# Kernel tuning notes

Hardware: AMD Instinct MI355X
Metric: run time of the kernel (lower is better)

Reference implementation:

```python
import jax, jax.numpy as jnp
import numpy as np

B, L, H, LH = 512, 128, 768, 256  # batch, max_seq_len, bert hidden, lstm hidden


def setup_inputs() -> dict:
    key = jax.random.key(0)
    ks = jax.random.split(key, 12)
    def rn(k, shape, s=0.02):
        return jax.random.normal(k, shape, dtype=jnp.float32) * s
    return {
        "x": jax.random.normal(ks[0], (B, L, H), dtype=jnp.float32),  # summed BERT layers 8:
        "w_ih": rn(ks[1], (4 * LH, H)),
        "w_hh": rn(ks[2], (4 * LH, LH)),
        "b_ih": jnp.zeros((4 * LH,), jnp.float32),
        "b_hh": jnp.zeros((4 * LH,), jnp.float32),
        "conv1_w": rn(ks[3], (256, H, 7)),   # Conv2d(1,256,(7,768)) == 1D conv, in=768
        "conv1_b": jnp.zeros((256,), jnp.float32),
        "conv2_w": rn(ks[4], (64, 256, 5)),
        "conv2_b": jnp.zeros((64,), jnp.float32),
        "conv3_w": rn(ks[5], (256, 64, 3)),
        "conv3_b": jnp.zeros((256,), jnp.float32),
        "conv4_w": rn(ks[6], (16, 256, 1)),
        "conv4_b": jnp.zeros((16,), jnp.float32),
        "fc1_w": rn(ks[7], (128, LH + 2 * L)),  # lstm_hidden + cnn_feature_size
        "fc1_b": jnp.zeros((128,), jnp.float32),
        "fc2_w": rn(ks[8], (32, 128)),
        "fc2_b": jnp.zeros((32,), jnp.float32),
        "fc3_w": rn(ks[9], (2, 32)),
        "fc3_b": jnp.zeros((2,), jnp.float32),
    }


def _conv1d(x, w, b, pad):
    # x: [B, Cin, L], w: [Cout, Cin, K]
    y = jax.lax.conv_general_dilated(
        x, w, window_strides=(1,), padding=[(pad, pad)],
        dimension_numbers=("NCH", "OIH", "NCH"))
    return y + b[None, :, None]


def _pool2(x):
    # max_pool1d(kernel=2, stride=2)
    b, c, l = x.shape
    return x.reshape(b, c, l // 2, 2).max(-1)


def reference(x, w_ih, w_hh, b_ih, b_hh,
              conv1_w, conv1_b, conv2_w, conv2_b, conv3_w, conv3_b,
              conv4_w, conv4_b, fc1_w, fc1_b, fc2_w, fc2_b, fc3_w, fc3_b):
    bs = x.shape[0]
    # --- LSTMCell loop over time (PyTorch gate order: i, f, g, o) ---
    def step(carry, xt):
        hx, cx = carry
        gates = xt @ w_ih.T + b_ih + hx @ w_hh.T + b_hh
        i, f, g, o = jnp.split(gates, 4, axis=-1)
        cx = jax.nn.sigmoid(f) * cx + jax.nn.sigmoid(i) * jnp.tanh(g)
        hx = jax.nn.sigmoid(o) * jnp.tanh(cx)
        return (hx, cx), hx
    h0 = jnp.zeros((bs, LH), x.dtype)
    _, hxs = jax.lax.scan(step, (h0, h0), x.transpose(1, 0, 2))  # [L, B, LH]
    hx_mean = hxs.mean(0)  # [B, LH]
    # --- CNN stack (conv1 over seq with full-width kernel == 1D conv) ---
    xc = x.transpose(0, 2, 1)  # [B, 768, L]
    y = jax.nn.relu(_pool2(_conv1d(xc, conv1_w, conv1_b, 3)))  # [B,256,L/2]
    y = jax.nn.relu(_pool2(_conv1d(y, conv2_w, conv2_b, 2)))   # [B,64,L/4]
    y = jax.nn.relu(_pool2(_conv1d(y, conv3_w, conv3_b, 1)))   # [B,256,L/8]
    y = jax.nn.relu(_conv1d(y, conv4_w, conv4_b, 0))           # [B,16,L/8]
    y = y.reshape(bs, -1)  # [B, 2L]
    # --- MLP head ---
    z = jnp.concatenate([hx_mean, y], axis=1)
    z = jax.nn.relu(z @ fc1_w.T + fc1_b)
    z = jax.nn.relu(z @ fc2_w.T + fc2_b)
    return jax.nn.relu(z @ fc3_w.T + fc3_b)
```

## Files before the change

kernel.cpp:

```cpp
#include <hip/hip_runtime.h>

#define BB 512
#define LL 128
#define HH 768
#define LHID 256
#define TCHUNK 16
#define NCHUNK 8

typedef _Float16 h8 __attribute__((ext_vector_type(8)));
typedef _Float16 h4 __attribute__((ext_vector_type(4)));
typedef float f16acc __attribute__((ext_vector_type(16)));

#define APAD 72
#define XSP 50331648

__device__ __forceinline__ float fsig(float x) { return 1.f / (1.f + __expf(-x)); }
__device__ __forceinline__ float ftanh(float x) { return 1.f - 2.f / (__expf(2.f * x) + 1.f); }

__global__ __launch_bounds__(256) void xsplit_kernel(
    const float* __restrict__ x, _Float16* __restrict__ xs) {
  size_t e = ((size_t)blockIdx.x * 256 + threadIdx.x) * 8;
  float4 a = *(const float4*)&x[e];
  float4 b = *(const float4*)&x[e + 4];
  h8 hi, lo;
  hi[0] = (_Float16)a.x; lo[0] = (_Float16)(a.x - (float)hi[0]);
  hi[1] = (_Float16)a.y; lo[1] = (_Float16)(a.y - (float)hi[1]);
  hi[2] = (_Float16)a.z; lo[2] = (_Float16)(a.z - (float)hi[2]);
  hi[3] = (_Float16)a.w; lo[3] = (_Float16)(a.w - (float)hi[3]);
  hi[4] = (_Float16)b.x; lo[4] = (_Float16)(b.x - (float)hi[4]);
  hi[5] = (_Float16)b.y; lo[5] = (_Float16)(b.y - (float)hi[5]);
  hi[6] = (_Float16)b.z; lo[6] = (_Float16)(b.z - (float)hi[6]);
  hi[7] = (_Float16)b.w; lo[7] = (_Float16)(b.w - (float)hi[7]);
  *(h8*)&xs[e] = hi;
  *(h8*)&xs[XSP + e] = lo;
}

__global__ __launch_bounds__(256) void prep_kernel(
    const float* __restrict__ w_ih, const float* __restrict__ w_hh,
    const float* __restrict__ b_ih, const float* __restrict__ b_hh,
    const float* __restrict__ w1, const float* __restrict__ w2, const float* __restrict__ w3,
    const float* __restrict__ w4,
    const float* __restrict__ fc1_w, const float* __restrict__ fc2_w, const float* __restrict__ fc3_w,
    float* __restrict__ w_q, float* __restrict__ biasg,
    _Float16* __restrict__ w1s, _Float16* __restrict__ wihs,
    float* __restrict__ w2t, float* __restrict__ w3t, float* __restrict__ w4t,
    float* __restrict__ fc1_wt, float* __restrict__ fc2_wt, float* __restrict__ fc3_wt) {
  int tid = blockIdx.x * 256 + threadIdx.x;
  if (tid < 1376256) {
    int dk = tid / 196608, r = tid % 196608, co = r / 768, ci = r % 768;
    float v = w1[((size_t)co * 768 + ci) * 7 + dk] * 64.f;
    _Float16 h = (_Float16)v;
    w1s[tid] = h;
    w1s[1376256 + tid] = (_Float16)(v - (float)h);
  }
  if (tid < 786432) {
    int np = tid / 768, k = tid % 768;
    int u = np >> 2, gate = np & 3;
    float v = w_ih[(size_t)(gate * 256 + u) * 768 + k] * 64.f;
    _Float16 h = (_Float16)v;
    wihs[tid] = h;
    wihs[786432 + tid] = (_Float16)(v - (float)h);
  }
  if (tid < 65536) {
    int k = tid >> 8, t = tid & 255;
    float4 wv;
    wv.x = w_hh[(0 * 256 + t) * 256 + k];
    wv.y = w_hh[(1 * 256 + t) * 256 + k];
    wv.z = w_hh[(2 * 256 + t) * 256 + k];
    wv.w = w_hh[(3 * 256 + t) * 256 + k];
    *(float4*)&w_q[tid * 4] = wv;
  }
  if (tid < 1024) {
    int u = tid >> 2, gate = tid & 3;
    biasg[tid] = b_ih[gate * 256 + u] + b_hh[gate * 256 + u];
  }
  if (tid < 81920) {
    int ci = tid / 320, r = tid % 320, dk = r >> 6, co = r & 63;
    w2t[tid] = w2[(co * 256 + ci) * 5 + dk];
  }
  if (tid < 49152) {
    int ci = tid / 768, r = tid % 768, dk = r >> 8, co = r & 255;
    w3t[tid] = w3[(co * 64 + ci) * 3 + dk];
  }
  if (tid < 4096) {
    int ci = tid >> 4, co = tid & 15;
    w4t[tid] = w4[co * 256 + ci];
  }
  if (tid < 65536) {
    int k = tid >> 7, j = tid & 127;
    fc1_wt[tid] = fc1_w[j * 512 + k];
  }
  if (tid < 4096) {
    int k = tid >> 5, j = tid & 31;
    fc2_wt[tid] = fc2_w[j * 128 + k];
  }
  if (tid < 64) {
    int k = tid >> 1, j = tid & 1;
    fc3_wt[tid] = fc3_w[j * 32 + k];
  }
}

__global__ __launch_bounds__(256, 2) void gemm_gates_mfma(
    const _Float16* __restrict__ xs, const _Float16* __restrict__ wihs,
    const float* __restrict__ biasg, float* __restrict__ gates, int l0, int cmode) {
  __shared__ _Float16 Asp[2][128][APAD];
  __shared__ _Float16 Bsp[2][128][APAD];
  int tid = threadIdx.x;
  int gid = blockIdx.x;
  int mt = (gid & 7) + ((gid >> 6) << 3), nt = (gid >> 3) & 7;
  int m0 = mt << 7, n0 = nt << 7;
  int lane = tid & 63, w = tid >> 6;
  int wm = (w & 1) * 64, wn = (w >> 1) * 64;
  int r32 = lane & 31, hw8 = (lane >> 5) * 8;
  int g8 = (tid & 7) << 3;
  f16acc acc[2][2];
#pragma unroll
  for (int mm = 0; mm < 2; mm++)
#pragma unroll
    for (int nn = 0; nn < 2; nn++) acc[mm][nn] = (f16acc)(0.f);

  size_t abase[8], bbase[8];
#pragma unroll
  for (int i = 0; i < 8; i++) {
    int p = i >> 2, row = (i & 3) * 32 + (tid >> 3);
    int m = m0 + row;
    int xrow = cmode ? (((m >> 4) << 7) + l0 + (m & 15)) : m;
    abase[i] = (size_t)p * XSP + (size_t)xrow * 768 + g8;
    bbase[i] = (size_t)p * 786432 + (size_t)(n0 + row) * 768 + g8;
  }
  h8 ra[8], rb[8];
#pragma unroll
  for (int i = 0; i < 8; i++) {
    ra[i] = *(const h8*)&xs[abase[i]];
    rb[i] = *(const h8*)&wihs[bbase[i]];
  }

  for (int kc = 0; kc < 12; kc++) {
    if (kc) __syncthreads();
#pragma unroll
    for (int i = 0; i < 8; i++) {
      int p = i >> 2, row = (i & 3) * 32 + (tid >> 3);
      *(h8*)&Asp[p][row][g8] = ra[i];
      *(h8*)&Bsp[p][row][g8] = rb[i];
    }
    __syncthreads();
    if (kc < 11) {
      int k0 = (kc + 1) * 64;
#pragma unroll
      for (int i = 0; i < 8; i++) {
        ra[i] = *(const h8*)&xs[abase[i] + k0];
        rb[i] = *(const h8*)&wihs[bbase[i] + k0];
      }
    }
#pragma unroll
    for (int ks = 0; ks < 4; ks++) {
      int k = ks * 16 + hw8;
      h8 ah[2], al[2], bh[2], bl[2];
      ah[0] = *(const h8*)&Asp[0][wm + r32][k];
      ah[1] = *(const h8*)&Asp[0][wm + r32 + 32][k];
      al[0] = *(const h8*)&Asp[1][wm + r32][k];
      al[1] = *(const h8*)&Asp[1][wm + r32 + 32][k];
      bh[0] = *(const h8*)&Bsp[0][wn + r32][k];
      bh[1] = *(const h8*)&Bsp[0][wn + r32 + 32][k];
      bl[0] = *(const h8*)&Bsp[1][wn + r32][k];
      bl[1] = *(const h8*)&Bsp[1][wn + r32 + 32][k];
#pragma unroll
      for (int mm = 0; mm < 2; mm++)
#pragma unroll
        for (int nn = 0; nn < 2; nn++) {
          acc[mm][nn] = __builtin_amdgcn_mfma_f32_32x32x16_f16(ah[mm], bh[nn], acc[mm][nn], 0, 0, 0);
          acc[mm][nn] = __builtin_amdgcn_mfma_f32_32x32x16_f16(ah[mm], bl[nn], acc[mm][nn], 0, 0, 0);
          acc[mm][nn] = __builtin_amdgcn_mfma_f32_32x32x16_f16(al[mm], bh[nn], acc[mm][nn], 0, 0, 0);
        }
    }
  }
#pragma unroll
  for (int mm = 0; mm < 2; mm++)
#pragma unroll
    for (int nn = 0; nn < 2; nn++) {
      int n = n0 + wn + nn * 32 + r32;
      float bb = biasg[n];
#pragma unroll
      for (int reg = 0; reg < 16; reg++) {
        int row = (reg & 3) + 8 * (reg >> 2) + (hw8 >> 1);
        int m = m0 + wm + mm * 32 + row;
        gates[(size_t)m * 1024 + n] = acc[mm][nn][reg] * (1.f / 64.f) + bb;
      }
    }
}

__global__ __launch_bounds__(1024) void lstm_full(
    const float* __restrict__ gates, const float* __restrict__ w_q,
    float* __restrict__ z) {
  __shared__ float hl[4][256];
  __shared__ __align__(16) float ps[4][4][256][4];
  int tid = threadIdx.x;
  int t = tid & 255, q = tid >> 8;
  int r0 = blockIdx.x * 4;
  float c = 0.f, hs = 0.f;
  hl[q][t] = 0.f;
  __syncthreads();
  int kb = q << 6;
  for (int lc = 0; lc < 128; lc++) {
    float4 a[4];
#pragma unroll
    for (int r = 0; r < 4; r++) a[r] = make_float4(0.f, 0.f, 0.f, 0.f);
#pragma unroll 4
    for (int k = 0; k < 64; k++) {
      float4 wv = *(const float4*)&w_q[(size_t)(kb + k) * 1024 + t * 4];
#pragma unroll
      for (int r = 0; r < 4; r++) {
        float hv = hl[r][kb + k];
        a[r].x += hv * wv.x; a[r].y += hv * wv.y;
        a[r].z += hv * wv.z; a[r].w += hv * wv.w;
      }
    }
#pragma unroll
    for (int r = 0; r < 4; r++)
      *(float4*)&ps[q][r][t][0] = a[r];
    __syncthreads();
    float4 p0 = *(const float4*)&ps[0][q][t][0];
    float4 p1 = *(const float4*)&ps[1][q][t][0];
    float4 p2 = *(const float4*)&ps[2][q][t][0];
    float4 p3 = *(const float4*)&ps[3][q][t][0];
    float4 g4 = *(const float4*)&gates[((size_t)(r0 + q) * 128 + lc) * 1024 + t * 4];
    float gi = p0.x + p1.x + p2.x + p3.x + g4.x;
    float gf = p0.y + p1.y + p2.y + p3.y + g4.y;
    float gg = p0.z + p1.z + p2.z + p3.z + g4.z;
    float go = p0.w + p1.w + p2.w + p3.w + g4.w;
    float iv = fsig(gi), fv = fsig(gf), gv = ftanh(gg), ov = fsig(go);
    c = fv * c + iv * gv;
    float hv = ov * ftanh(c);
    hs += hv;
    hl[q][t] = hv;
    __syncthreads();
  }
  z[(size_t)(r0 + q) * 512 + t] = hs * (1.f / 128.f);
}

__global__ __launch_bounds__(512) void lstm_chunk(
    const float* __restrict__ gates, const float* __restrict__ w_q,
    float* __restrict__ h_state, float* __restrict__ c_state, float* __restrict__ hsum,
    float* __restrict__ z, int first, int last, int gB, int l0f) {
  __shared__ float hl[4][256];
  __shared__ __align__(16) float ps[4][256][4];
  int tid = threadIdx.x;
  int t = tid & 255, half = tid >> 8;
  int r0 = blockIdx.x * 4;
  int rown = half * 2, rother = 2 - rown;
  float c2[2], hs2[2];
#pragma unroll
  for (int rr = 0; rr < 2; rr++) {
    int r = rown + rr;
    float hv;
    if (first) { hv = 0.f; c2[rr] = 0.f; hs2[rr] = 0.f; }
    else {
      hv = h_state[(r0 + r) * 256 + t];
      c2[rr] = c_state[(r0 + r) * 256 + t];
      hs2[rr] = hsum[(r0 + r) * 256 + t];
    }
    hl[r][t] = hv;
  }
  __syncthreads();
  int kb = half << 7;
  for (int lc = 0; lc < TCHUNK; lc++) {
    float4 a[4];
#pragma unroll
    for (int r = 0; r < 4; r++) a[r] = make_float4(0.f, 0.f, 0.f, 0.f);
#pragma unroll 4
    for (int k = 0; k < 128; k++) {
      float4 wv = *(const float4*)&w_q[(size_t)(kb + k) * 1024 + t * 4];
#pragma unroll
      for (int r = 0; r < 4; r++) {
        float hv = hl[r][kb + k];
        a[r].x += hv * wv.x; a[r].y += hv * wv.y;
        a[r].z += hv * wv.z; a[r].w += hv * wv.w;
      }
    }
#pragma unroll
    for (int rr = 0; rr < 2; rr++)
      *(float4*)&ps[rother + rr][t][0] = a[rother + rr];
    __syncthreads();
    float hnew[2];
#pragma unroll
    for (int rr = 0; rr < 2; rr++) {
      int r = rown + rr;
      float4 p = *(const float4*)&ps[r][t][0];
      float4 g4 = *(const float4*)&gates[((size_t)(r0 + r) * gB + l0f + lc) * 1024 + t * 4];
      float gi = a[r].x + p.x + g4.x;
      float gf = a[r].y + p.y + g4.y;
      float gg = a[r].z + p.z + g4.z;
      float go = a[r].w + p.w + g4.w;
      float iv = fsig(gi), fv = fsig(gf), gv = ftanh(gg), ov = fsig(go);
      c2[rr] = fv * c2[rr] + iv * gv;
      float hv = ov * ftanh(c2[rr]);
      hs2[rr] += hv;
      hnew[rr] = hv;
    }
#pragma unroll
    for (int rr = 0; rr < 2; rr++) hl[rown + rr][t] = hnew[rr];
    __syncthreads();
  }
#pragma unroll
  for (int rr = 0; rr < 2; rr++) {
    int r = rown + rr;
    h_state[(r0 + r) * 256 + t] = hl[r][t];
    c_state[(r0 + r) * 256 + t] = c2[rr];
    hsum[(r0 + r) * 256 + t] = hs2[rr];
    if (last) z[(r0 + r) * 512 + t] = hs2[rr] * (1.f / 128.f);
  }
}

__global__ __launch_bounds__(256, 2) void conv1_mfma(
    const _Float16* __restrict__ xs, const _Float16* __restrict__ w1s,
    const float* __restrict__ b1, float* __restrict__ out1) {
  __shared__ _Float16 Asp[2][134][36];
  __shared__ _Float16 Bsp[2][64][228];
  int tid = threadIdx.x;
  int b = blockIdx.y;
  int co0 = blockIdx.x << 6;
  int lane = tid & 63, w = tid >> 6;
  int wm = (w & 1) * 64, wn = (w >> 1) * 32;
  int r32 = lane & 31, hw8 = (lane >> 5) * 8;
  f16acc acc[2];
  acc[0] = (f16acc)(0.f);
  acc[1] = (f16acc)(0.f);

  for (int cc = 0; cc < 24; cc++) {
    int ci0 = cc * 32;
    if (cc) __syncthreads();
    for (int f = tid; f < 1072; f += 256) {
      int p = f >= 536;
      int r = f - p * 536;
      int row = r >> 2, g = (r & 3) << 3;
      int l = row - 3;
      h8 v = (h8)(_Float16)0.f;
      if (l >= 0 && l < 128)
        v = *(const h8*)&xs[(size_t)p * XSP + ((size_t)b * 128 + l) * 768 + ci0 + g];
      *(h8*)&Asp[p][row][g] = v;
    }
    for (int f = tid; f < 3584; f += 256) {
      int p = f >= 1792;
      int r = f - p * 1792;
      int co = r / 28, gg = r - co * 28;
      int k = gg << 3;
      int dk = k >> 5, ci = k & 31;
      *(h8*)&Bsp[p][co][k] =
          *(const h8*)&w1s[(size_t)p * 1376256 + ((size_t)dk * 256 + co0 + co) * 768 + ci0 + ci];
    }
    __syncthreads();
#pragma unroll
    for (int ks = 0; ks < 14; ks++) {
      int dk = ks >> 1;
      int cib = ((ks & 1) << 4) + hw8;
      int kb = ks * 16 + hw8;
      h8 ah[2], al[2], bh, bl;
      ah[0] = *(const h8*)&Asp[0][wm + r32 + dk][cib];
      ah[1] = *(const h8*)&Asp[0][wm + 32 + r32 + dk][cib];
      al[0] = *(const h8*)&Asp[1][wm + r32 + dk][cib];
      al[1] = *(const h8*)&Asp[1][wm + 32 + r32 + dk][cib];
      bh = *(const h8*)&Bsp[0][wn + r32][kb];
      bl = *(const h8*)&Bsp[1][wn + r32][kb];
#pragma unroll
      for (int mm = 0; mm < 2; mm++) {
        acc[mm] = __builtin_amdgcn_mfma_f32_32x32x16_f16(ah[mm], bh, acc[mm], 0, 0, 0);
        acc[mm] = __builtin_amdgcn_mfma_f32_32x32x16_f16(ah[mm], bl, acc[mm], 0, 0, 0);
        acc[mm] = __builtin_amdgcn_mfma_f32_32x32x16_f16(al[mm], bh, acc[mm], 0, 0, 0);
      }
    }
  }
  int co = co0 + wn + r32;
  float bb = b1[co];
  size_t obase = ((size_t)b * 256 + co) * 64;
#pragma unroll
  for (int mm = 0; mm < 2; mm++) {
#pragma unroll
    for (int i = 0; i < 8; i++) {
      int rb = ((i & 1) << 1) + ((i >> 1) << 3) + (hw8 >> 1);
      float v = fmaxf(acc[mm][2 * i], acc[mm][2 * i + 1]) * (1.f / 64.f) + bb;
      out1[obase + ((wm + mm * 32 + rb) >> 1)] = fmaxf(v, 0.f);
    }
  }
}

__global__ __launch_bounds__(256) void conv2_kernel(
    const float* __restrict__ out1, const float* __restrict__ w2t,
    const float* __restrict__ b2, float* __restrict__ out2) {
  __shared__ float X2[32 * 68];
  __shared__ __align__(16) float W2[32 * 5 * 64];
  int tid = threadIdx.x;
  int b = blockIdx.x;
  int co = tid & 63, pg = tid >> 6;
  float acc[16] = {};
  for (int c0 = 0; c0 < 256; c0 += 32) {
    for (int f = tid; f < 512; f += 256) {
      int ci = f >> 4, q = (f & 15) << 2;
      float4 v = *(const float4*)&out1[(b * 256 + c0 + ci) * 64 + q];
      X2[ci * 68 + 2 + q + 0] = v.x; X2[ci * 68 + 2 + q + 1] = v.y;
      X2[ci * 68 + 2 + q + 2] = v.z; X2[ci * 68 + 2 + q + 3] = v.w;
    }
    if (tid < 32) { X2[tid * 68] = 0.f; X2[tid * 68 + 1] = 0.f; X2[tid * 68 + 66] = 0.f; X2[tid * 68 + 67] = 0.f; }
    for (int f = tid; f < 2560; f += 256)
      *(float4*)&W2[f * 4] = *(const float4*)&w2t[c0 * 320 + f * 4];
    __syncthreads();
    for (int ci = 0; ci < 32; ci++) {
      float xv[20];
#pragma unroll
      for (int u = 0; u < 20; u++) xv[u] = X2[ci * 68 + pg * 16 + u];
#pragma unroll
      for (int dk = 0; dk < 5; dk++) {
        float w = W2[(ci * 5 + dk) * 64 + co];
#pragma unroll
        for (int i = 0; i < 16; i++) acc[i] += xv[i + dk] * w;
      }
    }
    __syncthreads();
  }
  float bb = b2[co];
#pragma unroll
  for (int p = 0; p < 8; p++) {
    float v = fmaxf(acc[2 * p], acc[2 * p + 1]) + bb;
    out2[(b * 64 + co) * 32 + pg * 8 + p] = fmaxf(v, 0.f);
  }
}

__global__ __launch_bounds__(256) void conv3_kernel(
    const float* __restrict__ out2, const float* __restrict__ w3t,
    const float* __restrict__ b3, float* __restrict__ out3) {
  __shared__ float X3[64 * 34];
  __shared__ __align__(16) float W3[16 * 3 * 256];
  int tid = threadIdx.x;
  int b = blockIdx.x;
  float acc[32] = {};
  for (int f = tid; f < 512; f += 256) {
    int ci = f >> 3, q = (f & 7) << 2;
    float4 v = *(const float4*)&out2[(b * 64 + ci) * 32 + q];
    X3[ci * 34 + 1 + q + 0] = v.x; X3[ci * 34 + 1 + q + 1] = v.y;
    X3[ci * 34 + 1 + q + 2] = v.z; X3[ci * 34 + 1 + q + 3] = v.w;
  }
  if (tid < 64) { X3[tid * 34] = 0.f; X3[tid * 34 + 33] = 0.f; }
  __syncthreads();
  for (int c0 = 0; c0 < 64; c0 += 16) {
    for (int f = tid; f < 3072; f += 256)
      *(float4*)&W3[f * 4] = *(const float4*)&w3t[c0 * 768 + f * 4];
    __syncthreads();
    for (int ci = 0; ci < 16; ci++) {
      float xv[34];
#pragma unroll
      for (int u = 0; u < 34; u++) xv[u] = X3[(c0 + ci) * 34 + u];
#pragma unroll
      for (int dk = 0; dk < 3; dk++) {
        float w = W3[(ci * 3 + dk) * 256 + tid];
#pragma unroll
        for (int i = 0; i < 32; i++) acc[i] += xv[i + dk] * w;
      }
    }
    __syncthreads();
  }
  float bb = b3[tid];
#pragma unroll
  for (int p = 0; p < 16; p++) {
    float v = fmaxf(acc[2 * p], acc[2 * p + 1]) + bb;
    out3[(b * 256 + tid) * 16 + p] = fmaxf(v, 0.f);
  }
}

__global__ __launch_bounds__(256) void conv4_kernel(
    const float* __restrict__ out3, const float* __restrict__ w4t,
    const float* __restrict__ b4, float* __restrict__ z) {
  __shared__ __align__(16) float X4[256 * 16];
  __shared__ __align__(16) float W4[256 * 16];
  int tid = threadIdx.x;
  int b = blockIdx.x;
  for (int f = tid; f < 1024; f += 256) {
    *(float4*)&X4[f * 4] = *(const float4*)&out3[b * 4096 + f * 4];
    *(float4*)&W4[f * 4] = *(const float4*)&w4t[f * 4];
  }
  __syncthreads();
  int co = tid >> 4, l = tid & 15;
  float acc = 0.f;
#pragma unroll 8
  for (int ci = 0; ci < 256; ci++) acc += X4[ci * 16 + l] * W4[ci * 16 + co];
  z[b * 512 + 256 + tid] = fmaxf(acc + b4[co], 0.f);
}

__global__ __launch_bounds__(128) void head_kernel(
    const float* __restrict__ z,
    const float* __restrict__ fc1_wt, const float* __restrict__ fc1_b,
    const float* __restrict__ fc2_wt, const float* __restrict__ fc2_b,
    const float* __restrict__ fc3_wt, const float* __restrict__ fc3_b,
    float* __restrict__ out) {
  __shared__ __align__(16) float zs[512];
  __shared__ float h1[128];
  __shared__ float h2[32];
  int tid = threadIdx.x;
  int b = blockIdx.x;
  *(float4*)&zs[tid * 4] = *(const float4*)&z[b * 512 + tid * 4];
  __syncthreads();
  float acc = 0.f;
#pragma unroll 8
  for (int k = 0; k < 512; k++) acc += zs[k] * fc1_wt[k * 128 + tid];
  h1[tid] = fmaxf(acc + fc1_b[tid], 0.f);
  __syncthreads();
  if (tid < 32) {
    float a2 = 0.f;
#pragma unroll 8
    for (int k = 0; k < 128; k++) a2 += h1[k] * fc2_wt[k * 32 + tid];
    h2[tid] = fmaxf(a2 + fc2_b[tid], 0.f);
  }
  __syncthreads();
  if (tid < 2) {
    float a3 = 0.f;
#pragma unroll
    for (int k = 0; k < 32; k++) a3 += h2[k] * fc3_wt[k * 2 + tid];
    out[b * 2 + tid] = fmaxf(a3 + fc3_b[tid], 0.f);
  }
}

extern "C" void kernel_launch(void* const* d_in, const int* in_sizes, int n_in,
                              void* d_out, int out_size, void* d_ws, size_t ws_size,
                              hipStream_t stream) {
  const float* x     = (const float*)d_in[0];
  const float* w_ih  = (const float*)d_in[1];
  const float* w_hh  = (const float*)d_in[2];
  const float* b_ih  = (const float*)d_in[3];
  const float* b_hh  = (const float*)d_in[4];
  const float* w1    = (const float*)d_in[5];
  const float* b1    = (const float*)d_in[6];
  const float* w2    = (const float*)d_in[7];
  const float* b2    = (const float*)d_in[8];
  const float* w3    = (const float*)d_in[9];
  const float* b3    = (const float*)d_in[10];
  const float* w4    = (const float*)d_in[11];
  const float* b4    = (const float*)d_in[12];
  const float* fc1_w = (const float*)d_in[13];
  const float* fc1_b = (const float*)d_in[14];
  const float* fc2_w = (const float*)d_in[15];
  const float* fc2_b = (const float*)d_in[16];
  const float* fc3_w = (const float*)d_in[17];
  const float* fc3_b = (const float*)d_in[18];
  float* out = (float*)d_out;

  const size_t gfull = (size_t)65536 * 1024, gchunk = (size_t)8192 * 1024;
  const size_t xsf = (size_t)XSP;
  const size_t rest = 262144 + 1024 + 3 * 131072 + 262144 + 8388608 + 1048576 +
                      2097152 + 81920 + 49152 + 4096 + 65536 + 4096 + 64 + 786432;
  int full = (ws_size >= (gfull + xsf + rest) * 4) ? 1 : 0;
  size_t gsz = full ? gfull : gchunk;

  float* W = (float*)d_ws;
  size_t o = 0;
  float* gates  = W + o; o += gsz;
  float* w_q    = W + o; o += 262144;
  float* biasg  = W + o; o += 1024;
  float* h_st   = W + o; o += 131072;
  float* c_st   = W + o; o += 131072;
  float* hsum   = W + o; o += 131072;
  float* z      = W + o; o += 262144;
  float* out1   = W + o; o += (size_t)512 * 256 * 64;
  float* out2   = W + o; o += (size_t)512 * 64 * 32;
  float* out3   = W + o; o += (size_t)512 * 256 * 16;
  float* w2t    = W + o; o += 81920;
  float* w3t    = W + o; o += 49152;
  float* w4t    = W + o; o += 4096;
  float* fc1_wt = W + o; o += 65536;
  float* fc2_wt = W + o; o += 4096;
  float* fc3_wt = W + o; o += 64;
  _Float16* wihs = (_Float16*)(W + o); o += 786432;
  _Float16* xs   = (_Float16*)(W + o); o += xsf;
  _Float16* w1s = (_Float16*)out3;
  (void)in_sizes; (void)n_in; (void)out_size;

  xsplit_kernel<<<24576, 256, 0, stream>>>(x, xs);
  prep_kernel<<<5376, 256, 0, stream>>>(w_ih, w_hh, b_ih, b_hh, w1, w2, w3, w4,
                                        fc1_w, fc2_w, fc3_w,
                                        w_q, biasg, w1s, wihs, w2t, w3t, w4t,
                                        fc1_wt, fc2_wt, fc3_wt);
  if (full) {
    gemm_gates_mfma<<<4096, 256, 0, stream>>>(xs, wihs, biasg, gates, 0, 0);
    lstm_full<<<128, 1024, 0, stream>>>(gates, w_q, z);
  } else {
    for (int c = 0; c < NCHUNK; c++) {
      gemm_gates_mfma<<<512, 256, 0, stream>>>(xs, wihs, biasg, gates, c * TCHUNK, 1);
      lstm_chunk<<<128, 512, 0, stream>>>(gates, w_q, h_st, c_st, hsum, z,
                                          c == 0, c == NCHUNK - 1, 16, 0);
    }
  }
  conv1_mfma<<<dim3(4, 512), 256, 0, stream>>>(xs, w1s, b1, out1);
  conv2_kernel<<<512, 256, 0, stream>>>(out1, w2t, b2, out2);
  conv3_kernel<<<512, 256, 0, stream>>>(out2, w3t, b3, out3);
  conv4_kernel<<<512, 256, 0, stream>>>(out3, w4t, b4, z);
  head_kernel<<<512, 128, 0, stream>>>(z, fc1_wt, fc1_b, fc2_wt, fc2_b, fc3_wt, fc3_b, out);
}
```

Measured before the change: 3.107 ms.

## Prefetch conv1 tiles into registers and transpose LSTM hidden-state shared layout

In conv1_mfma, the global loads for the next channel chunk are issued into registers right after the shared-memory barrier, so they overlap the MFMA work on the current chunk. Address math is hoisted out of the loop and the zero padding rows are written once at the start. In lstm_full, the hidden state is stored transposed so each k step reads one float4 from shared memory instead of four scalars. The register prefetch raises VGPR pressure under launch_bounds(256,2), which could cost occupancy or cause spills.

After: 2.604 ms. 16.2% less time.

```diff
diff --git a/kernel.cpp b/kernel.cpp
--- a/kernel.cpp
+++ b/kernel.cpp
@@ -192,13 +192,13 @@
 __global__ __launch_bounds__(1024) void lstm_full(
     const float* __restrict__ gates, const float* __restrict__ w_q,
     float* __restrict__ z) {
-  __shared__ float hl[4][256];
+  __shared__ __align__(16) float hT[256][4];
   __shared__ __align__(16) float ps[4][4][256][4];
   int tid = threadIdx.x;
   int t = tid & 255, q = tid >> 8;
   int r0 = blockIdx.x * 4;
   float c = 0.f, hs = 0.f;
-  hl[q][t] = 0.f;
+  hT[t][q] = 0.f;
   __syncthreads();
   int kb = q << 6;
   for (int lc = 0; lc < 128; lc++) {
@@ -208,12 +208,11 @@
 #pragma unroll 4
     for (int k = 0; k < 64; k++) {
       float4 wv = *(const float4*)&w_q[(size_t)(kb + k) * 1024 + t * 4];
-#pragma unroll
-      for (int r = 0; r < 4; r++) {
-        float hv = hl[r][kb + k];
-        a[r].x += hv * wv.x; a[r].y += hv * wv.y;
-        a[r].z += hv * wv.z; a[r].w += hv * wv.w;
-      }
+      float4 hv = *(const float4*)&hT[kb + k][0];
+      a[0].x += hv.x * wv.x; a[0].y += hv.x * wv.y; a[0].z += hv.x * wv.z; a[0].w += hv.x * wv.w;
+      a[1].x += hv.y * wv.x; a[1].y += hv.y * wv.y; a[1].z += hv.y * wv.z; a[1].w += hv.y * wv.w;
+      a[2].x += hv.z * wv.x; a[2].y += hv.z * wv.y; a[2].z += hv.z * wv.z; a[2].w += hv.z * wv.w;
+      a[3].x += hv.w * wv.x; a[3].y += hv.w * wv.y; a[3].z += hv.w * wv.z; a[3].w += hv.w * wv.w;
     }
 #pragma unroll
     for (int r = 0; r < 4; r++)
@@ -232,7 +231,7 @@
     c = fv * c + iv * gv;
     float hv = ov * ftanh(c);
     hs += hv;
-    hl[q][t] = hv;
+    hT[t][q] = hv;
     __syncthreads();
   }
   z[(size_t)(r0 + q) * 512 + t] = hs * (1.f / 128.f);
@@ -314,7 +313,7 @@
 __global__ __launch_bounds__(256, 2) void conv1_mfma(
     const _Float16* __restrict__ xs, const _Float16* __restrict__ w1s,
     const float* __restrict__ b1, float* __restrict__ out1) {
-  __shared__ _Float16 Asp[2][134][36];
+  __shared__ _Float16 Asp[2][136][36];
   __shared__ _Float16 Bsp[2][64][228];
   int tid = threadIdx.x;
   int b = blockIdx.y;
@@ -326,29 +325,61 @@
   acc[0] = (f16acc)(0.f);
   acc[1] = (f16acc)(0.f);
 
+  if (tid < 64) {
+    int p = tid >= 32;
+    int r = tid & 31;
+    int rr = r >> 2;
+    int row = (rr < 3) ? rr : (128 + rr);
+    int g = (r & 3) << 3;
+    *(h8*)&Asp[p][row][g] = (h8)(_Float16)0.f;
+  }
+
+  size_t abase[4], bbase[14];
+  int adst_row[4], adst_g[4], bdst_p[14], bdst_co[14], bdst_k[14];
+#pragma unroll
+  for (int i = 0; i < 4; i++) {
+    int f = tid + 256 * i;
+    int p = f >> 9, r = f & 511;
+    int l = r >> 2, g = (r & 3) << 3;
+    adst_row[i] = 3 + l; adst_g[i] = g;
+    abase[i] = (size_t)(f >> 9) * XSP + ((size_t)b * 128 + l) * 768 + g;
+    (void)p;
+  }
+#pragma unroll
+  for (int i = 0; i < 14; i++) {
+    int f = tid + 256 * i;
+    int p = f >= 1792;
+    int r = f - p * 1792;
+    int co = r / 28, j = r - co * 28;
+    int k = j << 3;
+    int dk = k >> 5, ci = k & 31;
+    bdst_p[i] = p; bdst_co[i] = co; bdst_k[i] = k;
+    bbase[i] = (size_t)p * 1376256 + ((size_t)dk * 256 + co0 + co) * 768 + ci;
+  }
+  h8 ra[4], rb[14];
+#pragma unroll
+  for (int i = 0; i < 4; i++) ra[i] = *(const h8*)&xs[abase[i]];
+#pragma unroll
+  for (int i = 0; i < 14; i++) rb[i] = *(const h8*)&w1s[bbase[i]];
+
   for (int cc = 0; cc < 24; cc++) {
-    int ci0 = cc * 32;
     if (cc) __syncthreads();
-    for (int f = tid; f < 1072; f += 256) {
-      int p = f >= 536;
-      int r = f - p * 536;
-      int row = r >> 2, g = (r & 3) << 3;
-      int l = row - 3;
-      h8 v = (h8)(_Float16)0.f;
-      if (l >= 0 && l < 128)
-        v = *(const h8*)&xs[(size_t)p * XSP + ((size_t)b * 128 + l) * 768 + ci0 + g];
-      *(h8*)&Asp[p][row][g] = v;
-    }
-    for (int f = tid; f < 3584; f += 256) {
-      int p = f >= 1792;
-      int r = f - p * 1792;
-      int co = r / 28, gg = r - co * 28;
-      int k = gg << 3;
-      int dk = k >> 5, ci = k & 31;
-      *(h8*)&Bsp[p][co][k] =
-          *(const h8*)&w1s[(size_t)p * 1376256 + ((size_t)dk * 256 + co0 + co) * 768 + ci0 + ci];
-    }
-    __syncthreads();
+#pragma unroll
+    for (int i = 0; i < 4; i++) {
+      int f = tid + 256 * i;
+      *(h8*)&Asp[f >> 9][adst_row[i]][adst_g[i]] = ra[i];
+    }
+#pragma unroll
+    for (int i = 0; i < 14; i++)
+      *(h8*)&Bsp[bdst_p[i]][bdst_co[i]][bdst_k[i]] = rb[i];
+    __syncthreads();
+    if (cc < 23) {
+      int off = (cc + 1) * 32;
+#pragma unroll
+      for (int i = 0; i < 4; i++) ra[i] = *(const h8*)&xs[abase[i] + off];
+#pragma unroll
+      for (int i = 0; i < 14; i++) rb[i] = *(const h8*)&w1s[bbase[i] + off];
+    }
 #pragma unroll
     for (int ks = 0; ks < 14; ks++) {
       int dk = ks >> 1;
@@ -376,9 +407,9 @@
   for (int mm = 0; mm < 2; mm++) {
 #pragma unroll
     for (int i = 0; i < 8; i++) {
-      int rb = ((i & 1) << 1) + ((i >> 1) << 3) + (hw8 >> 1);
+      int rb2 = ((i & 1) << 1) + ((i >> 1) << 3) + (hw8 >> 1);
       float v = fmaxf(acc[mm][2 * i], acc[mm][2 * i + 1]) * (1.f / 64.f) + bb;
-      out1[obase + ((wm + mm * 32 + rb) >> 1)] = fmaxf(v, 0.f);
+      out1[obase + ((wm + mm * 32 + rb2) >> 1)] = fmaxf(v, 0.f);
     }
   }
 }
```
